# Kernel tuning notes

Measured on AMD Instinct MI355X. Metric: run time of the kernel, lower is better.

The kernel has to match this reference:

```python
import jax, jax.numpy as jnp
import numpy as np

# LIF hyperparameters (from the torch module's `parameters` dict)
C = 1.0            # C_Osc
THR = 1.0          # v_Osc_threshold
BS = 256           # trials_per_stimulus
N = 512            # neurons_n
N_IN = 512         # n_in
TAU_SYN = 0.01     # tau_Osc_Ie
TAU_SYN_REC = 0.01 # tau_Osc_Irec
TAU_NEU = 0.02     # tau_Osc
GAIN_SYN = 1.0     # TDE_to_Osc_current
GAIN_SYN_REC = 0.5 # gain_syn_rec
DT = 0.001         # clock_sim
VR = 0.0           # reset_osc
I_MIN = 0.0        # I_minimum_osc
I_STEP = 0.01      # I_step_osc
REFRAC = 0.002     # refrac_Osc
REFR = REFRAC / DT # refractory period in steps
T = 500            # simulated timesteps


def spike(x):
    # SurrGradSpike.forward: hard threshold (surrogate grad only matters in bwd)
    return (x > 0.0).astype(x.dtype)


def setup_inputs() -> dict:
    key = jax.random.key(0)
    k1, k2, k3 = jax.random.split(key, 3)
    x = jax.random.uniform(k1, (T, BS, N_IN), dtype=jnp.float32)
    # train=True init: h1 ~ N(1, (std*0.5/sqrt(n_in))^2), r1 ~ N(0, same)
    std = 1.0 * 0.5 / np.sqrt(N_IN)
    h1 = 1.0 + std * jax.random.normal(k2, (N_IN, N), dtype=jnp.float32)
    r1 = std * jax.random.normal(k3, (N, N), dtype=jnp.float32)
    return {"x": x, "h1": h1, "r1": r1}


def reference(x, h1, r1):
    steady = I_MIN + I_STEP * jnp.arange(N, dtype=jnp.float32)  # [N]

    def step(state, x_t):
        V, Isyn, Irec, cnt, spk = state
        Isyn = Isyn - DT * Isyn / TAU_SYN + GAIN_SYN * (x_t @ h1)
        Irec = Irec - DT * Irec / TAU_SYN_REC + GAIN_SYN_REC * (spk @ r1)
        V = V + DT * (-V / TAU_NEU + (Isyn + Irec + steady) / C)
        V = jnp.maximum(V, 0.0)
        spk_new = spike(V - THR)
        cnt = REFR * spk_new + (1.0 - spk_new) * (cnt - 1.0)
        V = (1.0 - spk_new) * V * (cnt <= 0.0).astype(V.dtype) + spk_new * VR
        return (V, Isyn, Irec, cnt, spk_new), spk_new

    init = (
        jnp.ones((BS, N), jnp.float32),   # V
        jnp.zeros((BS, N), jnp.float32),  # Isyn
        jnp.zeros((BS, N), jnp.float32),  # Irec
        jnp.zeros((BS, N), jnp.float32),  # count_refr
        jnp.zeros((BS, N), jnp.float32),  # spk
    )
    _, spikes = jax.lax.scan(step, init, x)
    return spikes  # [T, BS, N]
```

## Files before the change

### kernel.cpp

```cpp
#include <hip/hip_runtime.h>

typedef __attribute__((ext_vector_type(8))) short short8;
typedef __attribute__((ext_vector_type(4))) float f32x4;

constexpr int BSZ = 256;
constexpr int NRN = 512;
constexpr int KIN = 512;
constexpr int TT  = 500;
constexpr int BM  = 128;
constexpr int BN  = 128;
constexpr int KT  = 32;
constexpr int NBLK = (TT * BSZ / BM) * (NRN / BN);
constexpr size_t WS_NEED = (size_t)2 * KIN * NRN * sizeof(unsigned short);

__device__ __forceinline__ unsigned short bf16rne(float f) {
    unsigned u = __float_as_uint(f);
    u += 0x7FFFu + ((u >> 16) & 1u);
    return (unsigned short)(u >> 16);
}
__device__ __forceinline__ float bf16f(unsigned short s) {
    return __uint_as_float(((unsigned)s) << 16);
}
__device__ __forceinline__ unsigned cvtpk(float a, float b) {
    unsigned r;
    asm("v_cvt_pk_bf16_f32 %0, %1, %2" : "=v"(r) : "v"(a), "v"(b));
    return r;
}

__global__ __launch_bounds__(512)
void split_h(const float* __restrict__ h1,
             unsigned short* __restrict__ wsH,
             unsigned short* __restrict__ wsL)
{
    const int k = blockIdx.x;
    const int n = threadIdx.x;
    const float v = h1[(size_t)k * NRN + n];
    const unsigned short h  = bf16rne(v);
    const unsigned short lo = bf16rne(v - bf16f(h));
    const int kt = k >> 5, koct = (k >> 3) & 3, i = k & 7;
    const int nb = n >> 7, nl = n & 127;
    const int byte = (kt * 4 + nb) * 8192 +
                     ((nl * 64 + koct * 16) ^ (((nl >> 1) & 3) << 4)) + i * 2;
    *reinterpret_cast<unsigned short*>((char*)wsH + byte) = h;
    *reinterpret_cast<unsigned short*>((char*)wsL + byte) = lo;
}

template<bool PS>
__global__ __launch_bounds__(256)
void lif_gemm(const float* __restrict__ x,
              const float* __restrict__ h1,
              const unsigned short* __restrict__ wsH,
              const unsigned short* __restrict__ wsL,
              float* __restrict__ out)
{
    __shared__ short AhS[BM * KT], AlS[BM * KT], BhS[BN * KT], BlS[BN * KT];

    const int tid  = threadIdx.x;
    const int l    = tid & 63;
    const int w    = tid >> 6;
    const int wm   = (w & 1) * 64;
    const int wn   = (w >> 1) * 64;
    const int lrow = l & 15;
    const int loct = l >> 4;

    const int nid = (blockIdx.x & 7) * (NBLK / 8) + (blockIdx.x >> 3);
    const size_t m0 = (size_t)(nid >> 2) * BM;
    const int    nb = nid & 3;
    const int    n0 = nb * BN;

    f32x4 acc[4][4];
    #pragma unroll
    for (int i = 0; i < 4; ++i)
        #pragma unroll
        for (int j = 0; j < 4; ++j) acc[i][j] = (f32x4)0.0f;

    for (int kt = 0; kt < KIN / KT; ++kt) {
        if (PS) {
            const float4* sH = reinterpret_cast<const float4*>(
                (const char*)wsH + (kt * 4 + nb) * 8192);
            const float4* sL = reinterpret_cast<const float4*>(
                (const char*)wsL + (kt * 4 + nb) * 8192);
            float4* dH = reinterpret_cast<float4*>(BhS);
            float4* dL = reinterpret_cast<float4*>(BlS);
            dH[tid]       = sH[tid];
            dH[256 + tid] = sH[256 + tid];
            dL[tid]       = sL[tid];
            dL[256 + tid] = sL[256 + tid];
        } else {
            #pragma unroll
            for (int u2 = 0; u2 < 2; ++u2) {
                const int u = u2 * 256 + tid;
                const int nl = u & 127, koct = u >> 7;
                short8 hh, hl;
                #pragma unroll
                for (int i = 0; i < 8; ++i) {
                    const float v = h1[(size_t)(kt * KT + koct * 8 + i) * NRN + n0 + nl];
                    const unsigned short h = bf16rne(v);
                    hh[i] = (short)h;
                    hl[i] = (short)bf16rne(v - bf16f(h));
                }
                const int byte = (nl * 64 + koct * 16) ^ (((nl >> 1) & 3) << 4);
                *reinterpret_cast<short8*>((char*)BhS + byte) = hh;
                *reinterpret_cast<short8*>((char*)BlS + byte) = hl;
            }
        }
        #pragma unroll
        for (int u4 = 0; u4 < 4; ++u4) {
            const int u = u4 * 256 + tid;
            const int row = u >> 3, slot = u & 7;
            const float4 xv = *reinterpret_cast<const float4*>(
                x + (m0 + row) * KIN + kt * KT + slot * 4);
            const unsigned h01 = cvtpk(xv.x, xv.y);
            const unsigned h23 = cvtpk(xv.z, xv.w);
            const float r0 = xv.x - __uint_as_float(h01 << 16);
            const float r1v = xv.y - __uint_as_float(h01 & 0xFFFF0000u);
            const float r2 = xv.z - __uint_as_float(h23 << 16);
            const float r3 = xv.w - __uint_as_float(h23 & 0xFFFF0000u);
            const unsigned l01 = cvtpk(r0, r1v);
            const unsigned l23 = cvtpk(r2, r3);
            const unsigned long long hb = (unsigned long long)h01 | ((unsigned long long)h23 << 32);
            const unsigned long long lb = (unsigned long long)l01 | ((unsigned long long)l23 << 32);
            const int byte = (row * 64 + slot * 8) ^ (((row >> 1) & 3) << 4);
            *reinterpret_cast<unsigned long long*>((char*)AhS + byte) = hb;
            *reinterpret_cast<unsigned long long*>((char*)AlS + byte) = lb;
        }
        __syncthreads();

        short8 ah[4], al[4], bh[4], bl[4];
        #pragma unroll
        for (int mi = 0; mi < 4; ++mi) {
            const int row  = wm + mi * 16 + lrow;
            const int byte = (row * 64 + loct * 16) ^ (((row >> 1) & 3) << 4);
            ah[mi] = *reinterpret_cast<const short8*>((const char*)AhS + byte);
            al[mi] = *reinterpret_cast<const short8*>((const char*)AlS + byte);
        }
        #pragma unroll
        for (int ni = 0; ni < 4; ++ni) {
            const int nn   = wn + ni * 16 + lrow;
            const int byte = (nn * 64 + loct * 16) ^ (((nn >> 1) & 3) << 4);
            bh[ni] = *reinterpret_cast<const short8*>((const char*)BhS + byte);
            bl[ni] = *reinterpret_cast<const short8*>((const char*)BlS + byte);
        }

        __builtin_amdgcn_s_setprio(1);
        #pragma unroll
        for (int mi = 0; mi < 4; ++mi)
            #pragma unroll
            for (int ni = 0; ni < 4; ++ni) {
                acc[mi][ni] = __builtin_amdgcn_mfma_f32_16x16x32_bf16(ah[mi], bh[ni], acc[mi][ni], 0, 0, 0);
                acc[mi][ni] = __builtin_amdgcn_mfma_f32_16x16x32_bf16(ah[mi], bl[ni], acc[mi][ni], 0, 0, 0);
                acc[mi][ni] = __builtin_amdgcn_mfma_f32_16x16x32_bf16(al[mi], bh[ni], acc[mi][ni], 0, 0, 0);
            }
        __builtin_amdgcn_s_setprio(0);
        __syncthreads();
    }

    #pragma unroll
    for (int mi = 0; mi < 4; ++mi)
        #pragma unroll
        for (int j = 0; j < 4; ++j) {
            const size_t row = m0 + wm + mi * 16 + loct * 4 + j;
            float* op = out + row * NRN + n0 + wn + lrow;
            #pragma unroll
            for (int ni = 0; ni < 4; ++ni)
                op[ni * 16] = acc[mi][ni][j];
        }
}

__global__ __launch_bounds__(512, 2)
void lif_scan(const float* __restrict__ r1,
              float* __restrict__ out)
{
    __shared__ unsigned long long smask[2][8];
    __shared__ unsigned long long flg[2];

    const int n  = threadIdx.x;
    const int b  = blockIdx.x;
    const int wv = n >> 6;
    const int ln = n & 63;
    const size_t row = (size_t)b * NRN + n;
    constexpr size_t STEP = (size_t)BSZ * NRN;

    if (n < 16) ((unsigned long long*)smask)[n] = 0ULL;
    if (n < 2)  flg[n] = 0ULL;

    double csum = 0.0;
    for (int j = 0; j < KIN; ++j)
        csum += (double)r1[(size_t)j * NRN + n];

    double V = 1.0, Is = 0.0, Ir = 0.0, cnt = 0.0;
    const double steady = 0.01 * (double)n;
    constexpr double kS = 0.1, kN = 0.05, DT = 0.001;

    float a0 = out[0 * STEP + row];
    float a1 = out[1 * STEP + row];
    float a2 = out[2 * STEP + row];
    float a3 = out[3 * STEP + row];
    __syncthreads();

#define LIF_STEP(T, AREG)                                                     \
    {                                                                         \
        const int t_ = (T);                                                   \
        const int p_ = t_ & 1;                                                \
        const unsigned long long f_ = flg[p_];          \
        double aR;                                                            \
        if (f_ == 0xFFFFFFFFFFFFFFFFULL) {                \
            aR = csum;                                                        \
        } else if (f_ == 0ULL) {                             \
            aR = 0.0;                                                         \
        } else {                                       \
            aR = 0.0;                                                         \
            _Pragma("unroll")                                                 \
            for (int w = 0; w < 8; ++w) {                                     \
                unsigned long long m_ = smask[p_][w];                         \
                while (m_) {                                 \
                    const int j = w * 64 + __builtin_ctzll(m_);               \
                    aR += (double)r1[(size_t)j * NRN + n];                    \
                    m_ &= m_ - 1;                                             \
                }                                                             \
            }                                                                 \
        }                                                                     \
        Is = Is - kS * Is + (double)(AREG);                 \
        Ir = Ir - kS * Ir + 0.5 * aR;                       \
        double Vn = V - kN * V + DT * (Is + Ir + steady);                     \
        Vn = fmax(Vn, 0.0);                                                   \
        const bool sp = (Vn - 1.0) > 0.0;                                     \
        cnt = sp ? 2.0 : (cnt - 1.0);                           \
        V = sp ? 0.0 : ((cnt <= 0.0) ? Vn : 0.0);                             \
        out[(size_t)t_ * STEP + row] = sp ? 1.0f : 0.0f;                      \
        const unsigned long long bal = __ballot(sp);                          \
        if (ln == 0) {                                                        \
            smask[p_ ^ 1][wv] = bal;                                          \
            const unsigned char fb =                                          \
                (bal == 0xFFFFFFFFFFFFFFFFULL) ? 0xFFu                        \
                : ((bal == 0ULL) ? 0x00u : 0x01u);                            \
            ((unsigned char*)&flg[p_ ^ 1])[wv] = fb;                          \
        }                                                                     \
        __syncthreads();                                                      \
    }

    for (int t4 = 0; t4 < TT; t4 += 4) {
        LIF_STEP(t4 + 0, a0)
        a0 = (t4 + 4 < TT) ? out[(size_t)(t4 + 4) * STEP + row] : 0.0f;
        LIF_STEP(t4 + 1, a1)
        a1 = (t4 + 5 < TT) ? out[(size_t)(t4 + 5) * STEP + row] : 0.0f;
        LIF_STEP(t4 + 2, a2)
        a2 = (t4 + 6 < TT) ? out[(size_t)(t4 + 6) * STEP + row] : 0.0f;
        LIF_STEP(t4 + 3, a3)
        a3 = (t4 + 7 < TT) ? out[(size_t)(t4 + 7) * STEP + row] : 0.0f;
    }
#undef LIF_STEP
}

extern "C" void kernel_launch(void* const* d_in, const int* in_sizes, int n_in,
                              void* d_out, int out_size, void* d_ws, size_t ws_size,
                              hipStream_t stream) {
    const float* x  = (const float*)d_in[0];
    const float* h1 = (const float*)d_in[1];
    const float* r1 = (const float*)d_in[2];
    float* out = (float*)d_out;
    (void)in_sizes; (void)n_in; (void)out_size;

    if (ws_size >= WS_NEED) {
        unsigned short* wsH = (unsigned short*)d_ws;
        unsigned short* wsL = wsH + (size_t)KIN * NRN;
        split_h<<<dim3(KIN), dim3(NRN), 0, stream>>>(h1, wsH, wsL);
        lif_gemm<true><<<dim3(NBLK), dim3(256), 0, stream>>>(x, h1, wsH, wsL, out);
    } else {
        lif_gemm<false><<<dim3(NBLK), dim3(256), 0, stream>>>(x, h1, nullptr, nullptr, out);
    }
    lif_scan<<<dim3(BSZ), dim3(512), 0, stream>>>(r1, out);
}
```

Before: 393.1 us.

## Speculate eight all-spiking LIF steps per barrier, fall back on mismatch

The LIF scan now processes timesteps in chunks of eight. When the previous step had every neuron in the block spiking, it speculatively runs all eight steps assuming full recurrent input (csum), with no per-step barrier. One ballot then checks that every neuron spiked at every step. If not, state is restored and the eight steps are redone one barrier at a time. Input prefetch is widened from four to eight steps. The gain depends on how often the input keeps every neuron saturated, and mispredicted chunks pay for both the speculative pass and the replay.

```diff
diff --git a/kernel.cpp b/kernel.cpp
--- a/kernel.cpp
+++ b/kernel.cpp
@@ -12,6 +12,7 @@
 constexpr int KT  = 32;
 constexpr int NBLK = (TT * BSZ / BM) * (NRN / BN);
 constexpr size_t WS_NEED = (size_t)2 * KIN * NRN * sizeof(unsigned short);
+constexpr unsigned long long FULLM = 0xFFFFFFFFFFFFFFFFULL;
 
 __device__ __forceinline__ unsigned short bf16rne(float f) {
     unsigned u = __float_as_uint(f);
@@ -173,6 +174,7 @@
 {
     __shared__ unsigned long long smask[2][8];
     __shared__ unsigned long long flg[2];
+    __shared__ unsigned long long vflg;
 
     const int n  = threadIdx.x;
     const int b  = blockIdx.x;
@@ -192,23 +194,22 @@
     const double steady = 0.01 * (double)n;
     constexpr double kS = 0.1, kN = 0.05, DT = 0.001;
 
-    float a0 = out[0 * STEP + row];
-    float a1 = out[1 * STEP + row];
-    float a2 = out[2 * STEP + row];
-    float a3 = out[3 * STEP + row];
+    float cur[8], nxt[8];
+    #pragma unroll
+    for (int i = 0; i < 8; ++i) cur[i] = out[(size_t)i * STEP + row];
     __syncthreads();
 
-#define LIF_STEP(T, AREG)                                                     \
+#define STD_STEP(T, AREG)                                                     \
     {                                                                         \
         const int t_ = (T);                                                   \
         const int p_ = t_ & 1;                                                \
-        const unsigned long long f_ = flg[p_];          \
+        const unsigned long long f_ = flg[p_];                                \
         double aR;                                                            \
-        if (f_ == 0xFFFFFFFFFFFFFFFFULL) {                \
+        if (f_ == FULLM) {                                                    \
             aR = csum;                                                        \
-        } else if (f_ == 0ULL) {                             \
+        } else if (f_ == 0ULL) {                                              \
             aR = 0.0;                                                         \
-        } else {                                       \
+        } else {                                                              \
             aR = 0.0;                                                         \
             _Pragma("unroll")                                                 \
             for (int w = 0; w < 8; ++w) {                                     \
@@ -232,24 +233,70 @@
         if (ln == 0) {                                                        \
             smask[p_ ^ 1][wv] = bal;                                          \
             const unsigned char fb =                                          \
-                (bal == 0xFFFFFFFFFFFFFFFFULL) ? 0xFFu                        \
-                : ((bal == 0ULL) ? 0x00u : 0x01u);                            \
+                (bal == FULLM) ? 0xFFu : ((bal == 0ULL) ? 0x00u : 0x01u);     \
             ((unsigned char*)&flg[p_ ^ 1])[wv] = fb;                          \
         }                                                                     \
         __syncthreads();                                                      \
     }
 
-    for (int t4 = 0; t4 < TT; t4 += 4) {
-        LIF_STEP(t4 + 0, a0)
-        a0 = (t4 + 4 < TT) ? out[(size_t)(t4 + 4) * STEP + row] : 0.0f;
-        LIF_STEP(t4 + 1, a1)
-        a1 = (t4 + 5 < TT) ? out[(size_t)(t4 + 5) * STEP + row] : 0.0f;
-        LIF_STEP(t4 + 2, a2)
-        a2 = (t4 + 6 < TT) ? out[(size_t)(t4 + 6) * STEP + row] : 0.0f;
-        LIF_STEP(t4 + 3, a3)
-        a3 = (t4 + 7 < TT) ? out[(size_t)(t4 + 7) * STEP + row] : 0.0f;
+    for (int t0 = 0; t0 < 496; t0 += 8) {
+        #pragma unroll
+        for (int i = 0; i < 8; ++i)
+            nxt[i] = (t0 + 8 + i < TT) ? out[(size_t)(t0 + 8 + i) * STEP + row] : 0.0f;
+
+        if (flg[t0 & 1] == FULLM) {
+            const double Vc = V, Isc = Is, Irc = Ir, cc = cnt;
+            bool allm = true;
+            #pragma unroll
+            for (int i = 0; i < 8; ++i) {
+                Is = Is - kS * Is + (double)cur[i];
+                Ir = Ir - kS * Ir + 0.5 * csum;
+                double Vn = V - kN * V + DT * (Is + Ir + steady);
+                Vn = fmax(Vn, 0.0);
+                const bool sp = (Vn - 1.0) > 0.0;
+                allm &= sp;
+                cnt = sp ? 2.0 : (cnt - 1.0);
+                V = sp ? 0.0 : ((cnt <= 0.0) ? Vn : 0.0);
+                out[(size_t)(t0 + i) * STEP + row] = sp ? 1.0f : 0.0f;
+            }
+            const unsigned long long bal = __ballot(allm);
+            if (ln == 0) {
+                ((unsigned char*)&vflg)[wv] = (bal == FULLM) ? 0xFFu : 0x00u;
+                smask[t0 & 1][wv] = FULLM;
+                ((unsigned char*)&flg[t0 & 1])[wv] = 0xFFu;
+            }
+            __syncthreads();
+            if (vflg != FULLM) {
+                V = Vc; Is = Isc; Ir = Irc; cnt = cc;
+                STD_STEP(t0 + 0, cur[0])
+                STD_STEP(t0 + 1, cur[1])
+                STD_STEP(t0 + 2, cur[2])
+                STD_STEP(t0 + 3, cur[3])
+                STD_STEP(t0 + 4, cur[4])
+                STD_STEP(t0 + 5, cur[5])
+                STD_STEP(t0 + 6, cur[6])
+                STD_STEP(t0 + 7, cur[7])
+            }
+        } else {
+            STD_STEP(t0 + 0, cur[0])
+            STD_STEP(t0 + 1, cur[1])
+            STD_STEP(t0 + 2, cur[2])
+            STD_STEP(t0 + 3, cur[3])
+            STD_STEP(t0 + 4, cur[4])
+            STD_STEP(t0 + 5, cur[5])
+            STD_STEP(t0 + 6, cur[6])
+            STD_STEP(t0 + 7, cur[7])
+        }
+
+        #pragma unroll
+        for (int i = 0; i < 8; ++i) cur[i] = nxt[i];
     }
-#undef LIF_STEP
+
+    STD_STEP(496, cur[0])
+    STD_STEP(497, cur[1])
+    STD_STEP(498, cur[2])
+    STD_STEP(499, cur[3])
+#undef STD_STEP
 }
 
 extern "C" void kernel_launch(void* const* d_in, const int* in_sizes, int n_in,
```

Result: faster. 335.7 us (-14.6%).
